# Optimization experiments

Hardware: AMD Instinct MI355X
Metric: run time of the kernel (lower is better)

The kernel has to match this reference:

```python
import jax, jax.numpy as jnp
import numpy as np


def setup_inputs() -> dict:
    key = jax.random.key(0)
    k1, k2, k3, k4 = jax.random.split(key, 4)
    B, T, D = 32, 2048, 128
    queries = jax.random.normal(k1, (B, T, D), dtype=jnp.float32)
    keys = jax.random.normal(k2, (B, T, D), dtype=jnp.float32)
    values = jax.random.normal(k3, (B, T, D), dtype=jnp.float32)
    valid_lens = jax.random.randint(k4, (B,), 0, T, dtype=jnp.int32)
    return {"queries": queries, "keys": keys, "values": values, "valid_lens": valid_lens}


def reference(queries, keys, values, valid_lens):
    d = queries.shape[-1]
    scale = d / 0.5  # faithful to source: 2*d, NOT sqrt(d)
    # (B, Tq, Tk) scores
    scores = jnp.einsum('bqd,bkd->bqk', queries, keys) / scale
    T = scores.shape[-1]
    # lengths (B,) -> mask (B, 1, Tk), broadcast over query rows
    mask = jnp.arange(T) < valid_lens[:, None, None]
    neg_inf = jnp.finfo(scores.dtype).min
    logits = jnp.where(mask, scores, neg_inf)
    probs = jax.nn.softmax(logits, axis=-1)
    fully_masked = ~jnp.any(mask, axis=-1, keepdims=True)
    probs = jnp.where(fully_masked, jnp.zeros_like(probs), probs)
    # dropout p=0.0 -> identity
    return jnp.einsum('bqk,bkv->bqv', probs, values)
```

## Files before the change

### kernel.cpp

```cpp
#include <hip/hip_runtime.h>
#include <hip/hip_bf16.h>
#include <stdint.h>

#define B_ 32
#define T_ 2048
#define D_ 128
#define BQ 64
#define BK 32
#define NBUF 3

typedef __attribute__((ext_vector_type(8))) __bf16 bf16x8;
typedef __attribute__((ext_vector_type(16))) float f32x16;

__device__ __forceinline__ float fast_exp2(float x) {
#if __has_builtin(__builtin_amdgcn_exp2f)
    return __builtin_amdgcn_exp2f(x);
#else
    return exp2f(x);
#endif
}

__device__ __forceinline__ f32x16 zero16() {
    f32x16 z;
    #pragma unroll
    for (int i = 0; i < 16; ++i) z[i] = 0.f;
    return z;
}

__device__ __forceinline__ uint32_t pk2(float a, float b) {
    union { __hip_bfloat16 h; unsigned short u; } ua, ub;
    ua.h = __float2bfloat16(a); ub.h = __float2bfloat16(b);
    return (uint32_t)ua.u | ((uint32_t)ub.u << 16);
}

__device__ __forceinline__ void plswap(uint32_t& a, uint32_t& b) {
    asm("v_permlane32_swap_b32 %0, %1" : "+v"(a), "+v"(b));
}

__device__ __forceinline__ void gll16(const __hip_bfloat16* g, __hip_bfloat16* lds) {
    __builtin_amdgcn_global_load_lds(
        (const __attribute__((address_space(1))) uint32_t*)g,
        (__attribute__((address_space(3))) uint32_t*)lds,
        16, 0, 0);
}

__global__ __launch_bounds__(256, 2)
void prep(const float* __restrict__ K, const float* __restrict__ V,
          const int* __restrict__ vlens,
          __hip_bfloat16* __restrict__ Kb, __hip_bfloat16* __restrict__ VTb)
{
    __shared__ float tile[64][132];
    const int b = blockIdx.y, k0 = blockIdx.x * 64;
    const int kmax = (vlens[b] + 63) & ~63;
    if (k0 >= kmax) return;

    {
        const float4* src = (const float4*)(K + ((size_t)b * T_ + k0) * D_);
        uint2* dst = (uint2*)(Kb + ((size_t)b * T_ + k0) * D_);
        #pragma unroll
        for (int it = 0; it < 8; ++it) {
            int c = it * 256 + threadIdx.x;
            float4 v = src[c];
            union { __hip_bfloat16 h[4]; uint2 u; } pk;
            pk.h[0] = __float2bfloat16(v.x); pk.h[1] = __float2bfloat16(v.y);
            pk.h[2] = __float2bfloat16(v.z); pk.h[3] = __float2bfloat16(v.w);
            dst[c] = pk.u;
        }
    }

    {
        const float4* src = (const float4*)(V + ((size_t)b * T_ + k0) * D_);
        #pragma unroll
        for (int it = 0; it < 8; ++it) {
            int c = it * 256 + threadIdx.x;
            int row = c >> 5, c4 = c & 31;
            *(float4*)&tile[row][c4 * 4] = src[c];
        }
        __syncthreads();
        #pragma unroll
        for (int it = 0; it < 8; ++it) {
            int c = it * 256 + threadIdx.x;
            int kc = c & 15, d = c >> 4;
            union { __hip_bfloat16 h[4]; uint2 u; } pk;
            #pragma unroll
            for (int j = 0; j < 4; ++j) {
                int jj = (j + kc) & 3;
                pk.h[jj] = __float2bfloat16(tile[kc * 4 + jj][d]);
            }
            *(uint2*)(VTb + ((size_t)b * D_ + d) * T_ + k0 + kc * 4) = pk.u;
        }
    }
}

__global__ __launch_bounds__(128, 2)
void attn_main(const float* __restrict__ Q, const int* __restrict__ vlens,
               const __hip_bfloat16* __restrict__ Kb,
               const __hip_bfloat16* __restrict__ VTb,
               float* __restrict__ out)
{
    const int tid  = threadIdx.x;
    const int wave = tid >> 6;
    const int lane = tid & 63;
    const int l32  = lane & 31;
    const int hi   = lane >> 5;

    const int b    = blockIdx.y;
    const int q0   = blockIdx.x * BQ;
    const int vlen = vlens[b];
    const int nkb  = (vlen + BK - 1) / BK;

    __shared__ __hip_bfloat16 sK [NBUF][BK][128];
    __shared__ __hip_bfloat16 sVT[NBUF][128][BK];

    const float C = 1.4426950408889634f / 256.0f;

    bf16x8 qf[8];
    {
        const float* qp = Q + ((size_t)b * T_ + q0 + wave * 32 + l32) * D_ + hi * 8;
        #pragma unroll
        for (int ds = 0; ds < 8; ++ds) {
            const float4* p4 = (const float4*)(qp + ds * 16);
            float4 a = p4[0], c = p4[1];
            __hip_bfloat16 h[8] = {
                __float2bfloat16(a.x), __float2bfloat16(a.y),
                __float2bfloat16(a.z), __float2bfloat16(a.w),
                __float2bfloat16(c.x), __float2bfloat16(c.y),
                __float2bfloat16(c.z), __float2bfloat16(c.w) };
            qf[ds] = *(const bf16x8*)h;
        }
    }

    f32x16 o[4];
    #pragma unroll
    for (int dt = 0; dt < 4; ++dt) o[dt] = zero16();
    float lsum = 0.f;

    const __hip_bfloat16* kb_base = Kb  + (size_t)b * T_ * D_;
    const __hip_bfloat16* vt_base = VTb + (size_t)b * D_ * T_;

    auto stage = [&](int k0s, int buf) {
        #pragma unroll
        for (int it = 0; it < 4; ++it) {
            const int blk = wave * 4 + it;
            {
                const int row = blk * 4 + (lane >> 4);
                const int s   = (lane & 15) ^ (row & 7);
                gll16(kb_base + (size_t)(k0s + row) * D_ + s * 8,
                      &sK[buf][0][0] + blk * 512);
            }
            {
                const int row = blk * 16 + (lane >> 2);
                const int s   = (lane & 3) ^ ((row >> 1) & 3);
                gll16(vt_base + (size_t)row * T_ + k0s + s * 8,
                      &sVT[buf][0][0] + blk * 512);
            }
        }
    };

    if (nkb > 0) stage(0, 0);
    if (nkb > 1) {
        stage(BK, 1);
        asm volatile("s_waitcnt vmcnt(8)" ::: "memory");
    } else {
        asm volatile("s_waitcnt vmcnt(0)" ::: "memory");
    }
    __builtin_amdgcn_s_barrier();

    int cur = 0;
    for (int kb = 0; kb < nkb; ++kb) {
        const int k0 = kb * BK;

        if (kb + 2 < nkb) {
            int nxt2 = cur + 2; if (nxt2 >= NBUF) nxt2 -= NBUF;
            stage(k0 + 2 * BK, nxt2);
        }
        if (kb + 1 < nkb) asm volatile("s_waitcnt vmcnt(8)" ::: "memory");
        else              asm volatile("s_waitcnt vmcnt(0)" ::: "memory");
        __builtin_amdgcn_sched_barrier(0);

        f32x16 s0 = zero16();
        __builtin_amdgcn_s_setprio(1);
        #pragma unroll
        for (int ds = 0; ds < 8; ++ds) {
            bf16x8 kf = *(const bf16x8*)&sK[cur][l32][(((ds * 2 + hi) ^ (l32 & 7))) * 8];
            s0 = __builtin_amdgcn_mfma_f32_32x32x16_bf16(kf, qf[ds], s0, 0, 0, 0);
        }
        __builtin_amdgcn_s_setprio(0);

        bf16x8 pf[2];
        {
            const int kbase_l = k0 + 4 * hi;
            float p[16];
            #pragma unroll
            for (int r = 0; r < 16; ++r) {
                int krow = (r & 3) + 8 * (r >> 2);
                float e = fast_exp2(s0[r] * C);
                p[r] = (kbase_l + krow < vlen) ? e : 0.f;
            }
            lsum += (((p[0] + p[1]) + (p[2] + p[3])) + ((p[4] + p[5]) + (p[6] + p[7])))
                  + (((p[8] + p[9]) + (p[10] + p[11])) + ((p[12] + p[13]) + (p[14] + p[15])));
            #pragma unroll
            for (int k2 = 0; k2 < 2; ++k2) {
                const int base = k2 * 8;
                uint32_t A0 = pk2(p[base + 0], p[base + 1]);
                uint32_t B0 = pk2(p[base + 4], p[base + 5]);
                uint32_t A1 = pk2(p[base + 2], p[base + 3]);
                uint32_t B1 = pk2(p[base + 6], p[base + 7]);
                plswap(A0, B0);
                plswap(A1, B1);
                union { uint32_t u[4]; bf16x8 v; } fr;
                fr.u[0] = A0; fr.u[1] = A1; fr.u[2] = B0; fr.u[3] = B1;
                pf[k2] = fr.v;
            }
        }

        __builtin_amdgcn_s_setprio(1);
        #pragma unroll
        for (int ks = 0; ks < 2; ++ks)
            #pragma unroll
            for (int dt = 0; dt < 4; ++dt) {
                const int r = dt * 32 + l32;
                bf16x8 vf = *(const bf16x8*)&sVT[cur][r][(((ks * 2 + hi) ^ ((r >> 1) & 3))) * 8];
                o[dt] = __builtin_amdgcn_mfma_f32_32x32x16_bf16(pf[ks], vf, o[dt], 0, 0, 0);
            }
        __builtin_amdgcn_s_setprio(0);

        asm volatile("" ::: "memory");
        __builtin_amdgcn_s_barrier();
        cur = (cur == NBUF - 1) ? 0 : cur + 1;
    }

    float ls  = lsum + __shfl_xor(lsum, 32);
    float inv = (ls > 0.f) ? 1.0f / ls : 0.f;
    float invr[16];
    #pragma unroll
    for (int r = 0; r < 16; ++r)
        invr[r] = __shfl(inv, (r & 3) + 8 * (r >> 2) + 4 * hi);
    #pragma unroll
    for (int dt = 0; dt < 4; ++dt)
        #pragma unroll
        for (int r = 0; r < 16; ++r) {
            int q = (r & 3) + 8 * (r >> 2) + 4 * hi;
            out[((size_t)b * T_ + q0 + wave * 32 + q) * D_ + dt * 32 + l32]
                = o[dt][r] * invr[r];
        }
}

extern "C" void kernel_launch(void* const* d_in, const int* in_sizes, int n_in,
                              void* d_out, int out_size, void* d_ws, size_t ws_size,
                              hipStream_t stream) {
    const float* Q = (const float*)d_in[0];
    const float* K = (const float*)d_in[1];
    const float* V = (const float*)d_in[2];
    const int* vl  = (const int*)d_in[3];
    float* out     = (float*)d_out;

    const size_t kb_bytes = (size_t)B_ * T_ * D_ * 2;
    if (ws_size < 2 * kb_bytes) return;
    __hip_bfloat16* Kb  = (__hip_bfloat16*)d_ws;
    __hip_bfloat16* VTb = (__hip_bfloat16*)((char*)d_ws + kb_bytes);

    prep     <<<dim3(T_ / 64, B_), 256, 0, stream>>>(K, V, vl, Kb, VTb);
    attn_main<<<dim3(T_ / BQ, B_), 128, 0, stream>>>(Q, vl, Kb, VTb, out);
}
```

Baseline: 236.7 us.

## Double query tile to 4 waves, compute row sums via MFMA, simplify staging

Raises the query block from 64 to 128 rows with 256 threads, so each staged K/V tile is shared by four waves instead of two and per-block staging work is split further. The softmax denominator is now accumulated with an extra MFMA against a ones vector instead of scalar adds and cross-lane shuffles. The staging loop uses precomputed, incrementing pointers with fewer loads per wave, and the wait counts change to match. The cost is one extra MFMA per half-tile, plus fewer blocks and more registers per block, which may reduce occupancy.

```diff
diff --git a/kernel.cpp b/kernel.cpp
--- a/kernel.cpp
+++ b/kernel.cpp
@@ -5,7 +5,7 @@
 #define B_ 32
 #define T_ 2048
 #define D_ 128
-#define BQ 64
+#define BQ 128
 #define BK 32
 #define NBUF 3
 
@@ -92,7 +92,7 @@
     }
 }
 
-__global__ __launch_bounds__(128, 2)
+__global__ __launch_bounds__(256, 2)
 void attn_main(const float* __restrict__ Q, const int* __restrict__ vlens,
                const __hip_bfloat16* __restrict__ Kb,
                const __hip_bfloat16* __restrict__ VTb,
@@ -111,6 +111,8 @@
 
     __shared__ __hip_bfloat16 sK [NBUF][BK][128];
     __shared__ __hip_bfloat16 sVT[NBUF][128][BK];
+    __hip_bfloat16* sKf = &sK [0][0][0];
+    __hip_bfloat16* sVf = &sVT[0][0][0];
 
     const float C = 1.4426950408889634f / 256.0f;
 
@@ -130,38 +132,38 @@
         }
     }
 
+    bf16x8 ones;
+    #pragma unroll
+    for (int j = 0; j < 8; ++j) ones[j] = (__bf16)1.0f;
+
     f32x16 o[4];
     #pragma unroll
     for (int dt = 0; dt < 4; ++dt) o[dt] = zero16();
-    float lsum = 0.f;
+    f32x16 lacc = zero16();
 
     const __hip_bfloat16* kb_base = Kb  + (size_t)b * T_ * D_;
     const __hip_bfloat16* vt_base = VTb + (size_t)b * D_ * T_;
-
-    auto stage = [&](int k0s, int buf) {
-        #pragma unroll
-        for (int it = 0; it < 4; ++it) {
-            const int blk = wave * 4 + it;
-            {
-                const int row = blk * 4 + (lane >> 4);
-                const int s   = (lane & 15) ^ (row & 7);
-                gll16(kb_base + (size_t)(k0s + row) * D_ + s * 8,
-                      &sK[buf][0][0] + blk * 512);
-            }
-            {
-                const int row = blk * 16 + (lane >> 2);
-                const int s   = (lane & 3) ^ ((row >> 1) & 3);
-                gll16(vt_base + (size_t)row * T_ + k0s + s * 8,
-                      &sVT[buf][0][0] + blk * 512);
-            }
-        }
+    const int kr0 = (wave * 2 + 0) * 4 + (lane >> 4);
+    const int kr1 = (wave * 2 + 1) * 4 + (lane >> 4);
+    const int vr0 = (wave * 2 + 0) * 16 + (lane >> 2);
+    const int vr1 = (wave * 2 + 1) * 16 + (lane >> 2);
+    const __hip_bfloat16* kp0 = kb_base + (size_t)kr0 * D_ + (((lane & 15) ^ (kr0 & 7)) * 8);
+    const __hip_bfloat16* kp1 = kb_base + (size_t)kr1 * D_ + (((lane & 15) ^ (kr1 & 7)) * 8);
+    const __hip_bfloat16* vp0 = vt_base + (size_t)vr0 * T_ + (((lane & 3) ^ ((vr0 >> 1) & 3)) * 8);
+    const __hip_bfloat16* vp1 = vt_base + (size_t)vr1 * T_ + (((lane & 3) ^ ((vr1 >> 1) & 3)) * 8);
+
+    auto stage = [&](int buf) {
+        gll16(kp0, sKf + buf * (BK * 128) + (wave * 2 + 0) * 512); kp0 += (size_t)BK * D_;
+        gll16(vp0, sVf + buf * (128 * BK) + (wave * 2 + 0) * 512); vp0 += BK;
+        gll16(kp1, sKf + buf * (BK * 128) + (wave * 2 + 1) * 512); kp1 += (size_t)BK * D_;
+        gll16(vp1, sVf + buf * (128 * BK) + (wave * 2 + 1) * 512); vp1 += BK;
     };
 
-    if (nkb > 0) stage(0, 0);
+    if (nkb > 0) stage(0);
     if (nkb > 1) {
-        stage(BK, 1);
-        asm volatile("s_waitcnt vmcnt(8)" ::: "memory");
-    } else {
+        stage(1);
+        asm volatile("s_waitcnt vmcnt(4)" ::: "memory");
+    } else if (nkb > 0) {
         asm volatile("s_waitcnt vmcnt(0)" ::: "memory");
     }
     __builtin_amdgcn_s_barrier();
@@ -171,10 +173,10 @@
         const int k0 = kb * BK;
 
         if (kb + 2 < nkb) {
-            int nxt2 = cur + 2; if (nxt2 >= NBUF) nxt2 -= NBUF;
-            stage(k0 + 2 * BK, nxt2);
-        }
-        if (kb + 1 < nkb) asm volatile("s_waitcnt vmcnt(8)" ::: "memory");
+            int tb = cur + 2; if (tb >= NBUF) tb -= NBUF;
+            stage(tb);
+        }
+        if (kb + 2 < nkb) asm volatile("s_waitcnt vmcnt(4)" ::: "memory");
         else              asm volatile("s_waitcnt vmcnt(0)" ::: "memory");
         __builtin_amdgcn_sched_barrier(0);
 
@@ -197,8 +199,6 @@
                 float e = fast_exp2(s0[r] * C);
                 p[r] = (kbase_l + krow < vlen) ? e : 0.f;
             }
-            lsum += (((p[0] + p[1]) + (p[2] + p[3])) + ((p[4] + p[5]) + (p[6] + p[7])))
-                  + (((p[8] + p[9]) + (p[10] + p[11])) + ((p[12] + p[13]) + (p[14] + p[15])));
             #pragma unroll
             for (int k2 = 0; k2 < 2; ++k2) {
                 const int base = k2 * 8;
@@ -216,13 +216,15 @@
 
         __builtin_amdgcn_s_setprio(1);
         #pragma unroll
-        for (int ks = 0; ks < 2; ++ks)
+        for (int ks = 0; ks < 2; ++ks) {
+            lacc = __builtin_amdgcn_mfma_f32_32x32x16_bf16(pf[ks], ones, lacc, 0, 0, 0);
             #pragma unroll
             for (int dt = 0; dt < 4; ++dt) {
                 const int r = dt * 32 + l32;
                 bf16x8 vf = *(const bf16x8*)&sVT[cur][r][(((ks * 2 + hi) ^ ((r >> 1) & 3))) * 8];
                 o[dt] = __builtin_amdgcn_mfma_f32_32x32x16_bf16(pf[ks], vf, o[dt], 0, 0, 0);
             }
+        }
         __builtin_amdgcn_s_setprio(0);
 
         asm volatile("" ::: "memory");
@@ -230,12 +232,9 @@
         cur = (cur == NBUF - 1) ? 0 : cur + 1;
     }
 
-    float ls  = lsum + __shfl_xor(lsum, 32);
-    float inv = (ls > 0.f) ? 1.0f / ls : 0.f;
     float invr[16];
     #pragma unroll
-    for (int r = 0; r < 16; ++r)
-        invr[r] = __shfl(inv, (r & 3) + 8 * (r >> 2) + 4 * hi);
+    for (int r = 0; r < 16; ++r) invr[r] = (lacc[r] > 0.f) ? 1.0f / lacc[r] : 0.f;
     #pragma unroll
     for (int dt = 0; dt < 4; ++dt)
         #pragma unroll
@@ -261,5 +260,5 @@
     __hip_bfloat16* VTb = (__hip_bfloat16*)((char*)d_ws + kb_bytes);
 
     prep     <<<dim3(T_ / 64, B_), 256, 0, stream>>>(K, V, vl, Kb, VTb);
-    attn_main<<<dim3(T_ / BQ, B_), 128, 0, stream>>>(Q, vl, Kb, VTb, out);
-}
+    attn_main<<<dim3(T_ / BQ, B_), 256, 0, stream>>>(Q, vl, Kb, VTb, out);
+}
```

Result: faster. 224.8 us (-5.0%).
